# Kernel optimization log

Measured on AMD Instinct MI355X. Metric: run time of the kernel, lower is better.

## Reference

```python
import jax, jax.numpy as jnp
import numpy as np

B, D, H, O, C, L = 16384, 1024, 1024, 256, 8, 3  # batch, input, hidden, output, num_classes, num_layers


def setup_inputs() -> dict:
    key = jax.random.key(0)
    ks = jax.random.split(key, 9)
    s_in = 1.0 / np.sqrt(D)
    s_h = 1.0 / np.sqrt(H)
    return {
        "x": jax.random.normal(ks[0], (B, D), jnp.float32),
        # classifier: Linear(D, C)
        "Wc": jax.random.normal(ks[1], (D, C), jnp.float32) * s_in,
        "bc": jnp.zeros((C,), jnp.float32),
        # per-branch first linear: Linear(D, H), stacked over C branches
        "W1": jax.random.normal(ks[2], (C, D, H), jnp.float32) * s_in,
        "b1": jnp.zeros((C, H), jnp.float32),
        # per-branch hidden linears: (num_layers-1) x Linear(H, H)
        "W2": jax.random.normal(ks[3], (C, L - 1, H, H), jnp.float32) * s_h,
        "b2": jnp.zeros((C, L - 1, H), jnp.float32),
        # per-branch output linear: Linear(H, O)
        "Wo": jax.random.normal(ks[4], (C, H, O), jnp.float32) * s_h,
        "bo": jnp.zeros((C, O), jnp.float32),
    }


def reference(x, Wc, bc, W1, b1, W2, b2, Wo, bo):
    # classifier logits: (B, C)
    logits = x @ Wc + bc
    # argmax routing (no target_bin given), clamped as in torch
    class_idx = jnp.clip(jnp.argmax(logits, axis=-1), 0, C - 1)
    one_hot = jax.nn.one_hot(class_idx, C, dtype=x.dtype)  # (B, C)
    # dense compute-all-branches, faithful to the torch module
    h = jax.nn.relu(jnp.einsum("bd,cdh->bch", x, W1) + b1)  # (B, C, H)
    for i in range(L - 1):
        h = jax.nn.relu(jnp.einsum("bch,chk->bck", h, W2[:, i]) + b2[:, i])
    outputs = jnp.einsum("bch,cho->bco", h, Wo) + bo  # (B, C, O)
    output = jnp.sum(one_hot[:, :, None] * outputs, axis=1)  # (B, O)
    return output, logits
```

## Files before the change

kernel.cpp:

```cpp
#include <hip/hip_runtime.h>
#include <stdint.h>

#define BB 16384
#define DD 1024
#define HH 1024
#define OO 256
#define CC 8

typedef unsigned short u16;
typedef __attribute__((ext_vector_type(4))) unsigned short u16x4;
typedef __attribute__((ext_vector_type(8))) short bf16x8;
typedef __attribute__((ext_vector_type(4))) float f32x4;

__device__ __forceinline__ u16 f2bf(float f) {
    union { float f; uint32_t u; } v; v.f = f;
    const uint32_t u = v.u;
    return (u16)((u + 0x7FFFu + ((u >> 16) & 1u)) >> 16);
}

#define GLDS16(g, l)                                                                   \
    __builtin_amdgcn_global_load_lds((const __attribute__((address_space(1))) void*)(g), \
                                     (__attribute__((address_space(3))) void*)(l), 16, 0, 0)

__global__ __launch_bounds__(256)
void transpose_bf16_kernel(const float* __restrict__ src, u16* __restrict__ dst,
                           int R, int Cc)
{
    __shared__ float t[32][33];
    const int tid = threadIdx.x;
    const int mat = blockIdx.z;
    const int r0 = blockIdx.y * 32, c0 = blockIdx.x * 32;
    {
        const int rr = tid >> 3, c4 = (tid & 7) * 4;
        const float4 v = *(const float4*)(src + ((size_t)mat * R + r0 + rr) * Cc + c0 + c4);
        t[rr][c4 + 0] = v.x; t[rr][c4 + 1] = v.y; t[rr][c4 + 2] = v.z; t[rr][c4 + 3] = v.w;
    }
    __syncthreads();
    {
        const int cc = tid >> 3, k4 = (tid & 7) * 4;
        u16x4 o;
        o[0] = f2bf(t[k4 + 0][cc]);
        o[1] = f2bf(t[k4 + 1][cc]);
        o[2] = f2bf(t[k4 + 2][cc]);
        o[3] = f2bf(t[k4 + 3][cc]);
        *(u16x4*)(dst + ((size_t)mat * Cc + c0 + cc) * R + r0 + k4) = o;
    }
}

__global__ __launch_bounds__(256)
void logits_kernel(const float* __restrict__ x, const float* __restrict__ Wc,
                   const float* __restrict__ bc, float* __restrict__ logits_out,
                   u16* __restrict__ x_bf16, int* __restrict__ class_idx,
                   int* __restrict__ hist)
{
    __shared__ float WcT[CC][DD];
    __shared__ int clsarr[16];
    const int tid = threadIdx.x;
    #pragma unroll
    for (int j = 0; j < 8; ++j) {
        const int f = tid + 256 * j;
        const float4 v = ((const float4*)Wc)[f];
        const int d = f >> 1, c = (f & 1) * 4;
        WcT[c + 0][d] = v.x; WcT[c + 1][d] = v.y; WcT[c + 2][d] = v.z; WcT[c + 3][d] = v.w;
    }
    __syncthreads();

    const int lane = tid & 63, wv = tid >> 6;
    const int row0 = blockIdx.x * 16 + wv * 4;

    float acc[4][8];
    #pragma unroll
    for (int r = 0; r < 4; ++r)
        #pragma unroll
        for (int c = 0; c < 8; ++c) acc[r][c] = 0.f;

    #pragma unroll
    for (int p = 0; p < 2; ++p) {
        float4 xv[2][4];
        #pragma unroll
        for (int rr = 0; rr < 2; ++rr) {
            const float4* xr = (const float4*)(x + (size_t)(row0 + 2 * p + rr) * DD);
            #pragma unroll
            for (int j = 0; j < 4; ++j) xv[rr][j] = xr[lane + 64 * j];
        }
        #pragma unroll
        for (int rr = 0; rr < 2; ++rr) {
            u16* xb = x_bf16 + (size_t)(row0 + 2 * p + rr) * DD;
            #pragma unroll
            for (int j = 0; j < 4; ++j) {
                const float4 v = xv[rr][j];
                u16x4 o; o[0] = f2bf(v.x); o[1] = f2bf(v.y); o[2] = f2bf(v.z); o[3] = f2bf(v.w);
                *(u16x4*)(xb + 4 * (lane + 64 * j)) = o;
            }
        }
        #pragma unroll
        for (int j = 0; j < 4; ++j) {
            const int f = lane + 64 * j;
            #pragma unroll
            for (int c = 0; c < 8; ++c) {
                const float4 w = *(const float4*)&WcT[c][4 * f];
                #pragma unroll
                for (int rr = 0; rr < 2; ++rr)
                    acc[2 * p + rr][c] += xv[rr][j].x * w.x + xv[rr][j].y * w.y
                                        + xv[rr][j].z * w.z + xv[rr][j].w * w.w;
            }
        }
    }

    #pragma unroll
    for (int off = 8; off < 64; off <<= 1)
        #pragma unroll
        for (int r = 0; r < 4; ++r)
            #pragma unroll
            for (int c = 0; c < 8; ++c)
                acc[r][c] += __shfl_xor(acc[r][c], off, 64);

    const int cls = lane >> 3;
    const float bcv = bc[cls];
    float s[4];
    #pragma unroll
    for (int r = 0; r < 4; ++r) {
        float v = acc[r][0];
        #pragma unroll
        for (int c = 1; c < 8; ++c) v = (cls == c) ? acc[r][c] : v;
        s[r] = v;
    }
    #pragma unroll
    for (int off = 1; off < 8; off <<= 1)
        #pragma unroll
        for (int r = 0; r < 4; ++r) s[r] += __shfl_xor(s[r], off, 64);
    #pragma unroll
    for (int r = 0; r < 4; ++r) s[r] += bcv;

    #pragma unroll
    for (int r = 0; r < 4; ++r)
        if ((lane & 7) == 0) logits_out[(size_t)(row0 + r) * CC + cls] = s[r];

    int idx[4] = {cls, cls, cls, cls};
    #pragma unroll
    for (int off = 8; off < 64; off <<= 1) {
        #pragma unroll
        for (int r = 0; r < 4; ++r) {
            const float ov = __shfl_xor(s[r], off, 64);
            const int oi = __shfl_xor(idx[r], off, 64);
            const bool take = (ov > s[r]) || (ov == s[r] && oi < idx[r]);
            s[r] = take ? ov : s[r];
            idx[r] = take ? oi : idx[r];
        }
    }
    if (lane == 0) {
        #pragma unroll
        for (int r = 0; r < 4; ++r) {
            class_idx[row0 + r] = idx[r];
            clsarr[wv * 4 + r] = idx[r];
        }
    }
    __syncthreads();
    if (tid < 64) {
        const int myc = (tid < 16) ? clsarr[tid] : -1;
        int h = 0;
        #pragma unroll
        for (int cc = 0; cc < 8; ++cc) {
            const int p = __popcll(__ballot(myc == cc));
            h = (tid == cc) ? p : h;
        }
        if (tid < 8) hist[blockIdx.x * 8 + tid] = h;
    }
}

__global__ __launch_bounds__(256)
void scan_kernel(const int* __restrict__ hist, int* __restrict__ offsets,
                 int* __restrict__ bb)
{
    const int t = threadIdx.x, c = t >> 5, g = t & 31;
    int sum = 0;
    #pragma unroll 4
    for (int i = 0; i < 32; ++i) sum += hist[(g * 32 + i) * 8 + c];
    int inc = sum;
    #pragma unroll
    for (int d = 1; d < 32; d <<= 1) {
        const int v = __shfl_up(inc, d, 32);
        if (g >= d) inc += v;
    }
    __shared__ int tot[8], offL[9];
    if (g == 31) tot[c] = inc;
    __syncthreads();
    if (t == 0) {
        int o = 0; offL[0] = 0; offsets[0] = 0;
        #pragma unroll
        for (int c8 = 0; c8 < 8; ++c8) {
            o += (tot[c8] + 127) & ~127;
            offL[c8 + 1] = o; offsets[c8 + 1] = o;
        }
    }
    __syncthreads();
    int base = offL[c] + (inc - sum);
    #pragma unroll 4
    for (int i = 0; i < 32; ++i) {
        const int b = g * 32 + i;
        bb[b * 8 + c] = base;
        base += hist[b * 8 + c];
    }
}

__global__ __launch_bounds__(256)
void scatter_kernel(const int* __restrict__ class_idx, const int* __restrict__ bb,
                    int* __restrict__ rowidx)
{
    const int r = blockIdx.x * 256 + threadIdx.x;
    const int c = class_idx[r];
    const int lane = threadIdx.x & 63;
    const int gl = lane & ~15;
    const unsigned long long before = (1ull << lane) - (1ull << gl);
    int rank = 0;
    #pragma unroll
    for (int cc = 0; cc < 8; ++cc) {
        const unsigned long long m = __ballot(c == cc);
        const int p = __popcll(m & before);
        rank = (c == cc) ? p : rank;
    }
    rowidx[bb[(r >> 4) * 8 + c] + rank] = r;
}

template<int NSTRIDE, bool GATHER_A, bool RELU, bool FINAL>
__global__ __launch_bounds__(256)
void gemm_kernel(const u16* __restrict__ Abase, const u16* __restrict__ Wbase,
                 size_t wclass_stride, const float* __restrict__ bias_base,
                 int bias_stride, const int* __restrict__ offsets,
                 const int* __restrict__ rowidx, u16* __restrict__ Hout,
                 float* __restrict__ Fout)
{
    __shared__ u16 sA[128 * 32];
    __shared__ u16 sB[128 * 32];
    const int tid = threadIdx.x;
    const int m0 = blockIdx.x * 128;
    if (m0 >= offsets[CC]) return;
    int c = 0;
    while (m0 >= offsets[c + 1]) ++c;
    const int n0 = blockIdx.y * 128;

    const int srow = tid >> 2;
    const int kc8 = (tid & 3) * 8;
    int sa0 = m0 + srow, sa1 = m0 + srow + 64;
    if (GATHER_A) {
        const int g0 = rowidx[sa0]; sa0 = (g0 < 0) ? 0 : g0;
        const int g1 = rowidx[sa1]; sa1 = (g1 < 0) ? 0 : g1;
    }
    const u16* gA0 = Abase + (size_t)sa0 * 1024 + kc8;
    const u16* gA1 = Abase + (size_t)sa1 * 1024 + kc8;
    const u16* Wcl = Wbase + (size_t)c * wclass_stride;
    const u16* gB0 = Wcl + (size_t)(n0 + srow) * 1024 + kc8;
    const u16* gB1 = Wcl + (size_t)(n0 + srow + 64) * 1024 + kc8;
    u16* lA0 = sA + tid * 8;
    u16* lA1 = sA + 2048 + tid * 8;
    u16* lB0 = sB + tid * 8;
    u16* lB1 = sB + 2048 + tid * 8;

    const int lane = tid & 63, wv = tid >> 6;
    const int wm = (wv & 1) * 64, wn = (wv >> 1) * 64;
    const int lr = lane & 15, lg = lane >> 4;
    const u16* fA = sA + (wm + lr) * 32 + lg * 8;
    const u16* fB = sB + (wn + lr) * 32 + lg * 8;

    f32x4 acc[4][4];
    #pragma unroll
    for (int i = 0; i < 4; ++i)
        #pragma unroll
        for (int j = 0; j < 4; ++j)
            acc[i][j] = (f32x4){0.f, 0.f, 0.f, 0.f};

    for (int kt = 0; kt < 32; ++kt) {
        const int kb = kt * 32;
        GLDS16(gA0 + kb, lA0);
        GLDS16(gA1 + kb, lA1);
        GLDS16(gB0 + kb, lB0);
        GLDS16(gB1 + kb, lB1);
        __syncthreads();
        bf16x8 af[4], bfr[4];
        #pragma unroll
        for (int i = 0; i < 4; ++i) {
            af[i]  = *(const bf16x8*)(fA + i * 16 * 32);
            bfr[i] = *(const bf16x8*)(fB + i * 16 * 32);
        }
        #pragma unroll
        for (int mi = 0; mi < 4; ++mi)
            #pragma unroll
            for (int ni = 0; ni < 4; ++ni)
                acc[mi][ni] = __builtin_amdgcn_mfma_f32_16x16x32_bf16(
                    af[mi], bfr[ni], acc[mi][ni], 0, 0, 0);
        __syncthreads();
    }

    const float* bp = bias_base + (size_t)c * bias_stride + n0 + wn + lr;
    #pragma unroll
    for (int ni = 0; ni < 4; ++ni) {
        const float bv = bp[ni * 16];
        const int col = n0 + wn + ni * 16 + lr;
        #pragma unroll
        for (int mi = 0; mi < 4; ++mi) {
            const int rb = m0 + wm + mi * 16 + lg * 4;
            #pragma unroll
            for (int q = 0; q < 4; ++q) {
                float v = acc[mi][ni][q] + bv;
                if (RELU) v = v > 0.f ? v : 0.f;
                if (FINAL) {
                    const int orow = rowidx[rb + q];
                    if (orow >= 0) Fout[(size_t)orow * NSTRIDE + col] = v;
                } else {
                    Hout[(size_t)(rb + q) * NSTRIDE + col] = f2bf(v);
                }
            }
        }
    }
}

extern "C" void kernel_launch(void* const* d_in, const int* in_sizes, int n_in,
                              void* d_out, int out_size, void* d_ws, size_t ws_size,
                              hipStream_t stream)
{
    const float* x  = (const float*)d_in[0];
    const float* Wc = (const float*)d_in[1];
    const float* bc = (const float*)d_in[2];
    const float* W1 = (const float*)d_in[3];
    const float* b1 = (const float*)d_in[4];
    const float* W2 = (const float*)d_in[5];
    const float* b2 = (const float*)d_in[6];
    const float* Wo = (const float*)d_in[7];
    const float* bo = (const float*)d_in[8];
    float* out    = (float*)d_out;
    float* logits = out + (size_t)BB * OO;

    char* ws = (char*)d_ws;
    constexpr size_t PADMAX = BB + CC * 128;
    constexpr int NLB = BB / 16;
    int* offsets   = (int*)(ws + 0);
    int* hist      = (int*)(ws + 64);
    int* bb        = (int*)(ws + 64 + NLB * 32);
    int* class_idx = (int*)(ws + 64 + 2 * NLB * 32);
    int* rowidx    = (int*)((char*)class_idx + (size_t)BB * 4);
    u16* x_bf16    = (u16*)((char*)rowidx + PADMAX * 4);
    u16* hA  = x_bf16 + (size_t)BB * DD;
    u16* hB  = hA + PADMAX * HH;
    u16* W1T = hB + PADMAX * HH;
    u16* W2T = W1T + (size_t)CC * DD * HH;
    u16* WoT = W2T + (size_t)CC * 2 * HH * HH;

    hipMemsetAsync(rowidx, 0xFF, PADMAX * 4, stream);

    transpose_bf16_kernel<<<dim3(32, 32, 8),  256, 0, stream>>>(W1, W1T, DD, HH);
    transpose_bf16_kernel<<<dim3(32, 32, 16), 256, 0, stream>>>(W2, W2T, HH, HH);
    transpose_bf16_kernel<<<dim3(8, 32, 8),   256, 0, stream>>>(Wo, WoT, HH, OO);

    logits_kernel<<<NLB, 256, 0, stream>>>(x, Wc, bc, logits, x_bf16, class_idx, hist);
    scan_kernel<<<1, 256, 0, stream>>>(hist, offsets, bb);
    scatter_kernel<<<BB / 256, 256, 0, stream>>>(class_idx, bb, rowidx);

    constexpr int MT = BB / 128 + CC;
    gemm_kernel<HH, true,  true,  false><<<dim3(MT, 8), 256, 0, stream>>>(
        x_bf16, W1T, (size_t)DD * HH, b1, HH, offsets, rowidx, hA, nullptr);
    gemm_kernel<HH, false, true,  false><<<dim3(MT, 8), 256, 0, stream>>>(
        hA, W2T, (size_t)2 * HH * HH, b2, 2 * HH, offsets, rowidx, hB, nullptr);
    gemm_kernel<HH, false, true,  false><<<dim3(MT, 8), 256, 0, stream>>>(
        hB, W2T + (size_t)HH * HH, (size_t)2 * HH * HH, b2 + HH, 2 * HH, offsets, rowidx, hA, nullptr);
    gemm_kernel<OO, false, false, true ><<<dim3(MT, 2), 256, 0, stream>>>(
        hA, WoT, (size_t)OO * HH, bo, OO, offsets, rowidx, nullptr, out);
}
```

Measured before the change: 299.2 us.

## Double-buffer LDS tiles in grouped GEMM and remap blocks to XCDs

Switches the GEMM main loop to a two-stage LDS ping-pong, so the global-to-LDS loads for the next K tile are issued before the MFMAs on the current tile, with one barrier per iteration instead of two. It also flattens the 2D grid to 1D and remaps block ids so that consecutive logical tiles land on the same XCD, aiming for better L2 reuse of A rows and weight tiles. The cost is doubled LDS per block, which can lower occupancy, and the remap relies on the grid size being divisible by 8.

```diff
diff --git a/kernel.cpp b/kernel.cpp
--- a/kernel.cpp
+++ b/kernel.cpp
@@ -222,7 +222,32 @@
     rowidx[bb[(r >> 4) * 8 + c] + rank] = r;
 }
 
-template<int NSTRIDE, bool GATHER_A, bool RELU, bool FINAL>
+#define STAGE(b, kt)                            \
+    {                                           \
+        const int kb_ = (kt) * 32;              \
+        GLDS16(gA0 + kb_, lA0 + (b) * 4096);    \
+        GLDS16(gA1 + kb_, lA1 + (b) * 4096);    \
+        GLDS16(gB0 + kb_, lB0 + (b) * 4096);    \
+        GLDS16(gB1 + kb_, lB1 + (b) * 4096);    \
+    }
+
+#define COMPUTE(b)                                                        \
+    {                                                                     \
+        bf16x8 af[4], bfr[4];                                             \
+        _Pragma("unroll")                                                 \
+        for (int i = 0; i < 4; ++i) {                                     \
+            af[i]  = *(const bf16x8*)(fA + (b) * 4096 + i * 16 * 32);     \
+            bfr[i] = *(const bf16x8*)(fB + (b) * 4096 + i * 16 * 32);     \
+        }                                                                 \
+        _Pragma("unroll")                                                 \
+        for (int mi = 0; mi < 4; ++mi)                                    \
+            _Pragma("unroll")                                             \
+            for (int ni = 0; ni < 4; ++ni)                                \
+                acc[mi][ni] = __builtin_amdgcn_mfma_f32_16x16x32_bf16(    \
+                    af[mi], bfr[ni], acc[mi][ni], 0, 0, 0);               \
+    }
+
+template<int NT_Y, int NSTRIDE, bool GATHER_A, bool RELU, bool FINAL>
 __global__ __launch_bounds__(256)
 void gemm_kernel(const u16* __restrict__ Abase, const u16* __restrict__ Wbase,
                  size_t wclass_stride, const float* __restrict__ bias_base,
@@ -230,14 +255,17 @@
                  const int* __restrict__ rowidx, u16* __restrict__ Hout,
                  float* __restrict__ Fout)
 {
-    __shared__ u16 sA[128 * 32];
-    __shared__ u16 sB[128 * 32];
+    __shared__ u16 sA[2 * 128 * 32];
+    __shared__ u16 sB[2 * 128 * 32];
     const int tid = threadIdx.x;
-    const int m0 = blockIdx.x * 128;
+
+    const int bid = blockIdx.x;
+    const int wg = (bid & 7) * ((int)gridDim.x >> 3) + (bid >> 3);
+    const int m0 = (wg / NT_Y) * 128;
+    const int n0 = (wg % NT_Y) * 128;
     if (m0 >= offsets[CC]) return;
     int c = 0;
     while (m0 >= offsets[c + 1]) ++c;
-    const int n0 = blockIdx.y * 128;
 
     const int srow = tid >> 2;
     const int kc8 = (tid & 3) * 8;
@@ -269,27 +297,14 @@
         for (int j = 0; j < 4; ++j)
             acc[i][j] = (f32x4){0.f, 0.f, 0.f, 0.f};
 
-    for (int kt = 0; kt < 32; ++kt) {
-        const int kb = kt * 32;
-        GLDS16(gA0 + kb, lA0);
-        GLDS16(gA1 + kb, lA1);
-        GLDS16(gB0 + kb, lB0);
-        GLDS16(gB1 + kb, lB1);
+    STAGE(0, 0);
+    __syncthreads();
+    for (int kt = 0; kt < 31; ++kt) {
+        if (kt & 1) { STAGE(0, kt + 1); COMPUTE(1); }
+        else        { STAGE(1, kt + 1); COMPUTE(0); }
         __syncthreads();
-        bf16x8 af[4], bfr[4];
-        #pragma unroll
-        for (int i = 0; i < 4; ++i) {
-            af[i]  = *(const bf16x8*)(fA + i * 16 * 32);
-            bfr[i] = *(const bf16x8*)(fB + i * 16 * 32);
-        }
-        #pragma unroll
-        for (int mi = 0; mi < 4; ++mi)
-            #pragma unroll
-            for (int ni = 0; ni < 4; ++ni)
-                acc[mi][ni] = __builtin_amdgcn_mfma_f32_16x16x32_bf16(
-                    af[mi], bfr[ni], acc[mi][ni], 0, 0, 0);
-        __syncthreads();
-    }
+    }
+    COMPUTE(1);
 
     const float* bp = bias_base + (size_t)c * bias_stride + n0 + wn + lr;
     #pragma unroll
@@ -356,12 +371,12 @@
     scatter_kernel<<<BB / 256, 256, 0, stream>>>(class_idx, bb, rowidx);
 
     constexpr int MT = BB / 128 + CC;
-    gemm_kernel<HH, true,  true,  false><<<dim3(MT, 8), 256, 0, stream>>>(
+    gemm_kernel<8, HH, true,  true,  false><<<dim3(MT * 8), 256, 0, stream>>>(
         x_bf16, W1T, (size_t)DD * HH, b1, HH, offsets, rowidx, hA, nullptr);
-    gemm_kernel<HH, false, true,  false><<<dim3(MT, 8), 256, 0, stream>>>(
+    gemm_kernel<8, HH, false, true,  false><<<dim3(MT * 8), 256, 0, stream>>>(
         hA, W2T, (size_t)2 * HH * HH, b2, 2 * HH, offsets, rowidx, hB, nullptr);
-    gemm_kernel<HH, false, true,  false><<<dim3(MT, 8), 256, 0, stream>>>(
+    gemm_kernel<8, HH, false, true,  false><<<dim3(MT * 8), 256, 0, stream>>>(
         hB, W2T + (size_t)HH * HH, (size_t)2 * HH * HH, b2 + HH, 2 * HH, offsets, rowidx, hA, nullptr);
-    gemm_kernel<OO, false, false, true ><<<dim3(MT, 2), 256, 0, stream>>>(
+    gemm_kernel<2, OO, false, false, true ><<<dim3(MT * 2), 256, 0, stream>>>(
         hA, WoT, (size_t)OO * HH, bo, OO, offsets, rowidx, nullptr, out);
 }
```

New measurement: 274.6 us (median of 2 runs). 8.2% less time.
